# Performance work log

Measured on AMD Instinct MI355X. Metric: run time of the kernel, lower is better.

## Reference

```python
import jax, jax.numpy as jnp
import numpy as np

N = 50000      # nodes
E = 800000     # edges
F_IN = 256     # input node features
H = 64         # hidden_dim
C = 10         # num_classes
G = 64         # graphs in batch


def setup_inputs() -> dict:
    key = jax.random.key(0)
    ks = jax.random.split(key, 10)
    x = jax.random.normal(ks[0], (N, F_IN), dtype=jnp.float32)
    edge_index = jax.random.randint(ks[1], (2, E), 0, N, dtype=jnp.int64)
    batch = jnp.sort(jax.random.randint(ks[2], (N,), 0, G, dtype=jnp.int64))
    def glorot(k, fan_in, fan_out):
        return jax.random.normal(k, (fan_in, fan_out), dtype=jnp.float32) / jnp.sqrt(jnp.float32(fan_in))
    return {
        "x": x,
        "edge_index": edge_index,
        "batch": batch,
        "W1": glorot(ks[3], F_IN, H), "b1": jnp.zeros((H,), jnp.float32),
        "W2": glorot(ks[4], H, H),    "b2": jnp.zeros((H,), jnp.float32),
        "W3": glorot(ks[5], H, H),    "b3": jnp.zeros((H,), jnp.float32),
        "lin_W": glorot(ks[6], H, C), "lin_b": jnp.zeros((C,), jnp.float32),
    }


def reference(x, edge_index, batch, W1, b1, W2, b2, W3, b3, lin_W, lin_b):
    src, dst = edge_index[0], edge_index[1]
    # GCN normalization with self-loops: deg counts (A + I) in-degree
    deg = jax.ops.segment_sum(jnp.ones((E,), x.dtype), dst, num_segments=N) + 1.0
    dis = jax.lax.rsqrt(deg)                       # deg^{-1/2}, [N]
    edge_norm = dis[src] * dis[dst]                # [E]
    self_norm = dis * dis                          # [N] (self-loop weight)

    def gcn_conv_relu(h, W, b):
        h = h @ W                                  # [N, H]
        msg = h[src] * edge_norm[:, None]          # gather + scale, [E, H]
        agg = jax.ops.segment_sum(msg, dst, num_segments=N)
        agg = agg + h * self_norm[:, None]         # self-loop contribution
        return jax.nn.relu(agg + b)                # dropout is identity in eval

    h = gcn_conv_relu(x, W1, b1)
    h = gcn_conv_relu(h, W2, b2)
    h = gcn_conv_relu(h, W3, b3)

    # global mean pool over graphs
    counts = jax.ops.segment_sum(jnp.ones((N,), h.dtype), batch, num_segments=G)
    pooled = jax.ops.segment_sum(h, batch, num_segments=G) / jnp.maximum(counts, 1.0)[:, None]
    return pooled @ lin_W + lin_b                  # [G, C]
```

## Files before the change

### kernel.cpp

```cpp
#include <hip/hip_runtime.h>

#define N_NODES 50000
#define N_EDGES 800000
#define F_INPUT 256
#define HDIM 64
#define NCLS 10
#define NGRAPH 64

#define BSHIFT 7
#define NBUCK 391
#define SCAP 4096

typedef float f32x4v __attribute__((ext_vector_type(4)));
typedef short bf16x8 __attribute__((ext_vector_type(8)));

union B8U { uint4 q; bf16x8 v; };

__device__ __forceinline__ float bflo(unsigned v) { return __uint_as_float(v << 16); }
__device__ __forceinline__ float bfhi(unsigned v) { return __uint_as_float(v & 0xFFFF0000u); }
__device__ __forceinline__ unsigned f2b2(float a, float b) {
    unsigned x = __float_as_uint(a); x = (x + 0x7FFF + ((x >> 16) & 1)) >> 16;
    unsigned y = __float_as_uint(b); y = (y + 0x7FFF + ((y >> 16) & 1)) >> 16;
    return x | (y << 16);
}

__device__ __forceinline__ void split2(float x0, float x1, unsigned& h, unsigned& l) {
    unsigned u0 = __float_as_uint(x0), u1 = __float_as_uint(x1);
    unsigned m0 = u0 & 0xFFFF0000u, m1 = u1 & 0xFFFF0000u;
    h = (u0 >> 16) | m1;
    float r0 = x0 - __uint_as_float(m0);
    float r1 = x1 - __uint_as_float(m1);
    l = (__float_as_uint(r0) >> 16) | (__float_as_uint(r1) & 0xFFFF0000u);
}

__global__ __launch_bounds__(256) void k_part(const int* __restrict__ src,
                                              const int* __restrict__ dst,
                                              int* __restrict__ bcnt,
                                              int* __restrict__ stage, int E) {
    __shared__ int cnt[NBUCK];
    __shared__ int base[NBUCK];
    const int tid = threadIdx.x;
    const int e0 = blockIdx.x * 4096;
    int pb[16], pv[16];
    for (int t = tid; t < NBUCK; t += 256) cnt[t] = 0;
    __syncthreads();
#pragma unroll
    for (int j = 0; j < 16; ++j) {
        int e = e0 + j * 256 + tid;
        if (e < E) {
            int s = src[e], d = dst[e];
            pb[j] = d >> BSHIFT;
            pv[j] = (s << BSHIFT) | (d & 127);
            atomicAdd(&cnt[pb[j]], 1);
        } else pb[j] = -1;
    }
    __syncthreads();
    for (int t = tid; t < NBUCK; t += 256) {
        int c = cnt[t];
        base[t] = c ? atomicAdd(&bcnt[t], c) : 0;
        cnt[t] = 0;
    }
    __syncthreads();
#pragma unroll
    for (int j = 0; j < 16; ++j) {
        if (pb[j] >= 0) {
            int r = base[pb[j]] + atomicAdd(&cnt[pb[j]], 1);
            if (r < SCAP) stage[pb[j] * SCAP + r] = pv[j];
        }
    }
}

__global__ __launch_bounds__(256) void k_csr(const int* __restrict__ stage,
                                             const int* __restrict__ bcnt,
                                             int* __restrict__ degi,
                                             float* __restrict__ dis,
                                             int* __restrict__ off,
                                             int* __restrict__ eadj, int n) {
    __shared__ int cnt[128];
    __shared__ int loc[128];
    __shared__ int lcur[128];
    __shared__ int ebuf[SCAP];
    const int b = blockIdx.x;
    const int tid = threadIdx.x;
    const int n0 = b << BSHIFT;
    const int nn = min(128, n - n0);
    const int sb = b * SCAP;
    const int len = min(bcnt[b], SCAP);
    if (tid < 128) cnt[tid] = 0;
    __syncthreads();
    for (int j = tid; j < len; j += 256) atomicAdd(&cnt[stage[sb + j] & 127], 1);
    __syncthreads();
    if (tid < nn) {
        int dg = cnt[tid];
        degi[n0 + tid] = dg;
        dis[n0 + tid] = rsqrtf((float)(dg + 1));
    }
    if (tid < 128) loc[tid] = cnt[tid];
    __syncthreads();
    for (int d = 1; d < 128; d <<= 1) {
        int x = 0;
        if (tid < 128 && tid >= d) x = loc[tid - d];
        __syncthreads();
        if (tid < 128) loc[tid] += x;
        __syncthreads();
    }
    if (tid < 128) {
        int ex = loc[tid] - cnt[tid];
        if (tid < nn) off[n0 + tid] = sb + ex;
        lcur[tid] = ex;
    }
    __syncthreads();
    for (int j = tid; j < len; j += 256) {
        int p = stage[sb + j];
        int rk = atomicAdd(&lcur[p & 127], 1);
        ebuf[rk] = p >> BSHIFT;
    }
    __syncthreads();
    for (int j = tid; j < len; j += 256) eadj[sb + j] = ebuf[j];
}

__global__ __launch_bounds__(256) void k_prepW(const float* __restrict__ W1,
                                               const float* __restrict__ W2,
                                               const float* __restrict__ W3,
                                               uint4* __restrict__ Bf1,
                                               uint4* __restrict__ Bf2,
                                               uint4* __restrict__ Bf3) {
    int s = blockIdx.x * 256 + threadIdx.x;
    const float* W; uint4* out; int local, KS;
    if (s < 2048)      { W = W1; out = Bf1; local = s;        KS = 8; }
    else if (s < 2560) { W = W2; out = Bf2; local = s - 2048; KS = 2; }
    else               { W = W3; out = Bf3; local = s - 2560; KS = 2; }
    const int lane = local & 63;
    const int t    = (local >> 6) & 3;
    const int ks   = local >> 8;
    const int kb   = ks * 32 + ((lane >> 4) << 3);
    const int col  = t * 16 + (lane & 15);
    unsigned h[4], l[4];
#pragma unroll
    for (int j = 0; j < 4; ++j) {
        float x0 = W[(size_t)(kb + 2 * j) * HDIM + col];
        float x1 = W[(size_t)(kb + 2 * j + 1) * HDIM + col];
        split2(x0, x1, h[j], l[j]);
    }
    out[(ks * 4 + t) * 64 + lane]          = make_uint4(h[0], h[1], h[2], h[3]);
    out[((KS + ks) * 4 + t) * 64 + lane]   = make_uint4(l[0], l[1], l[2], l[3]);
}

__global__ __launch_bounds__(256) void k_gemm_mf(const float* __restrict__ A,
                                                 const uint4* __restrict__ Bf,
                                                 unsigned short* __restrict__ C,
                                                 int n, int lda, int ktn) {
    const int tid = threadIdx.x;
    const int ln  = tid & 63;
    const int wv  = tid >> 6;
    const int m   = ln & 15;
    const int kg  = ln >> 4;
    const int grow = blockIdx.x * 64 + wv * 16 + m;
    const float* ar = A + (size_t)min(grow, n - 1) * lda + kg * 8;

    f32x4v acc[4];
#pragma unroll
    for (int t = 0; t < 4; ++t)
#pragma unroll
        for (int j = 0; j < 4; ++j) acc[t][j] = 0.0f;

    float4 c0 = *(const float4*)(ar);
    float4 c1 = *(const float4*)(ar + 4);

    for (int ks = 0; ks < ktn; ++ks) {
        const int kn = (ks + 1 < ktn) ? (ks + 1) * 32 : 0;
        float4 p0 = *(const float4*)(ar + kn);
        float4 p1 = *(const float4*)(ar + kn + 4);

        const uint4* bp = Bf + (size_t)ks * 256 + ln;
        const uint4* bq = Bf + (size_t)(ktn + ks) * 256 + ln;
        B8U bh0, bh1, bh2, bh3, bl0, bl1, bl2, bl3;
        bh0.q = bp[0];   bh1.q = bp[64];  bh2.q = bp[128]; bh3.q = bp[192];
        bl0.q = bq[0];   bl1.q = bq[64];  bl2.q = bq[128]; bl3.q = bq[192];

        B8U ah, al;
        split2(c0.x, c0.y, ah.q.x, al.q.x);
        split2(c0.z, c0.w, ah.q.y, al.q.y);
        split2(c1.x, c1.y, ah.q.z, al.q.z);
        split2(c1.z, c1.w, ah.q.w, al.q.w);

        acc[0] = __builtin_amdgcn_mfma_f32_16x16x32_bf16(bh0.v, ah.v, acc[0], 0, 0, 0);
        acc[1] = __builtin_amdgcn_mfma_f32_16x16x32_bf16(bh1.v, ah.v, acc[1], 0, 0, 0);
        acc[2] = __builtin_amdgcn_mfma_f32_16x16x32_bf16(bh2.v, ah.v, acc[2], 0, 0, 0);
        acc[3] = __builtin_amdgcn_mfma_f32_16x16x32_bf16(bh3.v, ah.v, acc[3], 0, 0, 0);
        acc[0] = __builtin_amdgcn_mfma_f32_16x16x32_bf16(bl0.v, ah.v, acc[0], 0, 0, 0);
        acc[1] = __builtin_amdgcn_mfma_f32_16x16x32_bf16(bl1.v, ah.v, acc[1], 0, 0, 0);
        acc[2] = __builtin_amdgcn_mfma_f32_16x16x32_bf16(bl2.v, ah.v, acc[2], 0, 0, 0);
        acc[3] = __builtin_amdgcn_mfma_f32_16x16x32_bf16(bl3.v, ah.v, acc[3], 0, 0, 0);
        acc[0] = __builtin_amdgcn_mfma_f32_16x16x32_bf16(bh0.v, al.v, acc[0], 0, 0, 0);
        acc[1] = __builtin_amdgcn_mfma_f32_16x16x32_bf16(bh1.v, al.v, acc[1], 0, 0, 0);
        acc[2] = __builtin_amdgcn_mfma_f32_16x16x32_bf16(bh2.v, al.v, acc[2], 0, 0, 0);
        acc[3] = __builtin_amdgcn_mfma_f32_16x16x32_bf16(bh3.v, al.v, acc[3], 0, 0, 0);

        c0 = p0; c1 = p1;
    }

    if (grow < n) {
#pragma unroll
        for (int t = 0; t < 4; ++t) {
            uint2 p;
            p.x = f2b2(acc[t][0], acc[t][1]);
            p.y = f2b2(acc[t][2], acc[t][3]);
            *(uint2*)(C + (size_t)grow * HDIM + t * 16 + kg * 4) = p;
        }
    }
}

__global__ __launch_bounds__(256) void k_gemm_mb(const unsigned short* __restrict__ A,
                                                 const uint4* __restrict__ Bf,
                                                 unsigned short* __restrict__ C, int n) {
    const int tid = threadIdx.x;
    const int ln  = tid & 63;
    const int wv  = tid >> 6;
    const int m   = ln & 15;
    const int kg  = ln >> 4;
    const int grow = blockIdx.x * 64 + wv * 16 + m;
    const unsigned short* ar = A + (size_t)min(grow, n - 1) * HDIM + kg * 8;

    f32x4v acc[4];
#pragma unroll
    for (int t = 0; t < 4; ++t)
#pragma unroll
        for (int j = 0; j < 4; ++j) acc[t][j] = 0.0f;

#pragma unroll
    for (int ks = 0; ks < 2; ++ks) {
        B8U af;
        af.q = *(const uint4*)(ar + ks * 32);
        const uint4* bp = Bf + ks * 256 + ln;
        const uint4* bq = Bf + (2 + ks) * 256 + ln;
        B8U bh0, bh1, bh2, bh3, bl0, bl1, bl2, bl3;
        bh0.q = bp[0];  bh1.q = bp[64];  bh2.q = bp[128]; bh3.q = bp[192];
        bl0.q = bq[0];  bl1.q = bq[64];  bl2.q = bq[128]; bl3.q = bq[192];

        acc[0] = __builtin_amdgcn_mfma_f32_16x16x32_bf16(bh0.v, af.v, acc[0], 0, 0, 0);
        acc[1] = __builtin_amdgcn_mfma_f32_16x16x32_bf16(bh1.v, af.v, acc[1], 0, 0, 0);
        acc[2] = __builtin_amdgcn_mfma_f32_16x16x32_bf16(bh2.v, af.v, acc[2], 0, 0, 0);
        acc[3] = __builtin_amdgcn_mfma_f32_16x16x32_bf16(bh3.v, af.v, acc[3], 0, 0, 0);
        acc[0] = __builtin_amdgcn_mfma_f32_16x16x32_bf16(bl0.v, af.v, acc[0], 0, 0, 0);
        acc[1] = __builtin_amdgcn_mfma_f32_16x16x32_bf16(bl1.v, af.v, acc[1], 0, 0, 0);
        acc[2] = __builtin_amdgcn_mfma_f32_16x16x32_bf16(bl2.v, af.v, acc[2], 0, 0, 0);
        acc[3] = __builtin_amdgcn_mfma_f32_16x16x32_bf16(bl3.v, af.v, acc[3], 0, 0, 0);
    }

    if (grow < n) {
#pragma unroll
        for (int t = 0; t < 4; ++t) {
            uint2 p;
            p.x = f2b2(acc[t][0], acc[t][1]);
            p.y = f2b2(acc[t][2], acc[t][3]);
            *(uint2*)(C + (size_t)grow * HDIM + t * 16 + kg * 4) = p;
        }
    }
}

__global__ __launch_bounds__(256) void k_gather_b(const unsigned short* __restrict__ h,
                                                  const int* __restrict__ off,
                                                  const int* __restrict__ degi,
                                                  const int* __restrict__ eadj,
                                                  const float* __restrict__ dis,
                                                  const float* __restrict__ bias,
                                                  unsigned short* __restrict__ out, int n) {
    int t = blockIdx.x * 256 + threadIdx.x;
    int i = t >> 3;
    if (i >= n) return;
    const int l8 = t & 7;
    const int q = l8 * 8;
    const int gb = (threadIdx.x & 63) & ~7;
    float di = dis[i];
    int e0 = off[i];
    int e1 = e0 + degi[i];
    float a0 = 0.f, a1 = 0.f, a2 = 0.f, a3 = 0.f, a4 = 0.f, a5 = 0.f, a6 = 0.f, a7 = 0.f;
    for (int base = e0; base < e1; base += 8) {
        const int myE = base + l8;
        int sv = 0; float wv = 0.f;
        if (myE < e1) { sv = eadj[myE]; wv = dis[sv] * di; }
        const int m = e1 - base;
#pragma unroll
        for (int j = 0; j < 8; ++j) {
            if (j < m) {
                int sj = __shfl(sv, gb + j, 64);
                float wj = __shfl(wv, gb + j, 64);
                uint4 u = *(const uint4*)(h + (size_t)sj * HDIM + q);
                a0 = fmaf(bflo(u.x), wj, a0); a1 = fmaf(bfhi(u.x), wj, a1);
                a2 = fmaf(bflo(u.y), wj, a2); a3 = fmaf(bfhi(u.y), wj, a3);
                a4 = fmaf(bflo(u.z), wj, a4); a5 = fmaf(bfhi(u.z), wj, a5);
                a6 = fmaf(bflo(u.w), wj, a6); a7 = fmaf(bfhi(u.w), wj, a7);
            }
        }
    }
    float sn = di * di;
    uint4 us = *(const uint4*)(h + (size_t)i * HDIM + q);
    float4 bl = *(const float4*)(bias + q);
    float4 bh = *(const float4*)(bias + q + 4);
    a0 = fmaxf(fmaf(bflo(us.x), sn, a0) + bl.x, 0.f);
    a1 = fmaxf(fmaf(bfhi(us.x), sn, a1) + bl.y, 0.f);
    a2 = fmaxf(fmaf(bflo(us.y), sn, a2) + bl.z, 0.f);
    a3 = fmaxf(fmaf(bfhi(us.y), sn, a3) + bl.w, 0.f);
    a4 = fmaxf(fmaf(bflo(us.z), sn, a4) + bh.x, 0.f);
    a5 = fmaxf(fmaf(bfhi(us.z), sn, a5) + bh.y, 0.f);
    a6 = fmaxf(fmaf(bflo(us.w), sn, a6) + bh.z, 0.f);
    a7 = fmaxf(fmaf(bfhi(us.w), sn, a7) + bh.w, 0.f);
    uint4 o;
    o.x = f2b2(a0, a1); o.y = f2b2(a2, a3);
    o.z = f2b2(a4, a5); o.w = f2b2(a6, a7);
    *(uint4*)(out + (size_t)i * HDIM + q) = o;
}

__global__ __launch_bounds__(256) void k_gather_pool(const unsigned short* __restrict__ h,
                                                     const int* __restrict__ off,
                                                     const int* __restrict__ degi,
                                                     const int* __restrict__ eadj,
                                                     const float* __restrict__ dis,
                                                     const float* __restrict__ bias,
                                                     const int* __restrict__ batch,
                                                     float* __restrict__ pooled, int n) {
    __shared__ float sp[NGRAPH][HDIM];
    const int tid = threadIdx.x;
    int t = blockIdx.x * 256 + tid;
    int i = t >> 3;
    const bool valid = (i < n);
    const int l8 = t & 7;
    int q = l8 * 8;
    const int gb = (tid & 63) & ~7;
    const int i0 = (blockIdx.x * 256) >> 3;
    const int i1 = min(i0 + 32, n);
    const int gmin = batch[min(i0, n - 1)];
    const int gmax = batch[i1 - 1];
    for (int j = tid; j < NGRAPH * HDIM; j += 256) ((float*)sp)[j] = 0.f;
    __syncthreads();
    if (valid) {
        float di = dis[i];
        int e0 = off[i];
        int e1 = e0 + degi[i];
        float a0 = 0.f, a1 = 0.f, a2 = 0.f, a3 = 0.f, a4 = 0.f, a5 = 0.f, a6 = 0.f, a7 = 0.f;
        for (int base = e0; base < e1; base += 8) {
            const int myE = base + l8;
            int sv = 0; float wv = 0.f;
            if (myE < e1) { sv = eadj[myE]; wv = dis[sv] * di; }
            const int m = e1 - base;
#pragma unroll
            for (int j = 0; j < 8; ++j) {
                if (j < m) {
                    int sj = __shfl(sv, gb + j, 64);
                    float wj = __shfl(wv, gb + j, 64);
                    uint4 u = *(const uint4*)(h + (size_t)sj * HDIM + q);
                    a0 = fmaf(bflo(u.x), wj, a0); a1 = fmaf(bfhi(u.x), wj, a1);
                    a2 = fmaf(bflo(u.y), wj, a2); a3 = fmaf(bfhi(u.y), wj, a3);
                    a4 = fmaf(bflo(u.z), wj, a4); a5 = fmaf(bfhi(u.z), wj, a5);
                    a6 = fmaf(bflo(u.w), wj, a6); a7 = fmaf(bfhi(u.w), wj, a7);
                }
            }
        }
        float sn = di * di;
        uint4 us = *(const uint4*)(h + (size_t)i * HDIM + q);
        float4 bl = *(const float4*)(bias + q);
        float4 bh = *(const float4*)(bias + q + 4);
        a0 = fmaxf(fmaf(bflo(us.x), sn, a0) + bl.x, 0.f);
        a1 = fmaxf(fmaf(bfhi(us.x), sn, a1) + bl.y, 0.f);
        a2 = fmaxf(fmaf(bflo(us.y), sn, a2) + bl.z, 0.f);
        a3 = fmaxf(fmaf(bfhi(us.y), sn, a3) + bl.w, 0.f);
        a4 = fmaxf(fmaf(bflo(us.z), sn, a4) + bh.x, 0.f);
        a5 = fmaxf(fmaf(bfhi(us.z), sn, a5) + bh.y, 0.f);
        a6 = fmaxf(fmaf(bflo(us.w), sn, a6) + bh.z, 0.f);
        a7 = fmaxf(fmaf(bfhi(us.w), sn, a7) + bh.w, 0.f);
        int g = batch[i];
        atomicAdd(&sp[g][q + 0], a0); atomicAdd(&sp[g][q + 1], a1);
        atomicAdd(&sp[g][q + 2], a2); atomicAdd(&sp[g][q + 3], a3);
        atomicAdd(&sp[g][q + 4], a4); atomicAdd(&sp[g][q + 5], a5);
        atomicAdd(&sp[g][q + 6], a6); atomicAdd(&sp[g][q + 7], a7);
    }
    __syncthreads();
    int rows = gmax - gmin + 1;
    for (int j = tid; j < rows * HDIM; j += 256) {
        int r = j >> 6, c = j & 63;
        float v = sp[gmin + r][c];
        if (v != 0.f) atomicAdd(&pooled[(gmin + r) * HDIM + c], v);
    }
}

__global__ __launch_bounds__(640) void k_head(const float* __restrict__ pooled,
                                              const int* __restrict__ batch,
                                              const float* __restrict__ linW,
                                              const float* __restrict__ linb,
                                              float* __restrict__ out, int n) {
    int t = threadIdx.x;
    if (t >= NGRAPH * NCLS) return;
    int g = t / NCLS;
    int c = t - g * NCLS;
    int lo = 0, hi = n;
    while (lo < hi) { int m = (lo + hi) >> 1; if (batch[m] < g) lo = m + 1; else hi = m; }
    int s = lo;
    lo = 0; hi = n;
    while (lo < hi) { int m = (lo + hi) >> 1; if (batch[m] < g + 1) lo = m + 1; else hi = m; }
    float inv = 1.0f / fmaxf((float)(lo - s), 1.0f);
    float acc = linb[c];
#pragma unroll
    for (int k = 0; k < HDIM; ++k)
        acc = fmaf(pooled[g * HDIM + k] * inv, linW[k * NCLS + c], acc);
    out[g * NCLS + c] = acc;
}

extern "C" void kernel_launch(void* const* d_in, const int* in_sizes, int n_in,
                              void* d_out, int out_size, void* d_ws, size_t ws_size,
                              hipStream_t stream) {
    (void)in_sizes; (void)n_in; (void)out_size; (void)ws_size;
    const float* x    = (const float*)d_in[0];
    const int*   ei   = (const int*)d_in[1];
    const int*   batch= (const int*)d_in[2];
    const float* W1   = (const float*)d_in[3];
    const float* b1   = (const float*)d_in[4];
    const float* W2   = (const float*)d_in[5];
    const float* b2   = (const float*)d_in[6];
    const float* W3   = (const float*)d_in[7];
    const float* b3   = (const float*)d_in[8];
    const float* linW = (const float*)d_in[9];
    const float* linb = (const float*)d_in[10];
    float* out = (float*)d_out;

    const int N = N_NODES, E = N_EDGES;
    const int* src = ei;
    const int* dst = ei + E;

    char* ws = (char*)d_ws;
    unsigned short* hA = (unsigned short*)ws; ws += (size_t)N * HDIM * 2;
    unsigned short* hB = (unsigned short*)ws; ws += (size_t)N * HDIM * 2;
    float* dis    = (float*)ws; ws += (size_t)N * 4;
    int*   eadj   = (int*)ws;   ws += (size_t)NBUCK * SCAP * 4;
    int*   stage  = (int*)ws;   ws += (size_t)NBUCK * SCAP * 4;
    int*   degi   = (int*)ws;   ws += (size_t)N * 4;
    int*   off    = (int*)ws;   ws += (size_t)N * 4;
    int*   bcnt   = (int*)ws;   ws += ((size_t)NBUCK * 4 + 15) & ~(size_t)15;
    float* pooled = (float*)ws; ws += (size_t)NGRAPH * HDIM * 4;
    uint4* Bf1    = (uint4*)ws; ws += (size_t)2 * 8 * 4 * 64 * 16;
    uint4* Bf2    = (uint4*)ws; ws += (size_t)2 * 2 * 4 * 64 * 16;
    uint4* Bf3    = (uint4*)ws; ws += (size_t)2 * 2 * 4 * 64 * 16;

    const int nbE = (E + 4095) / 4096;
    const int gb  = (N + 63) / 64;
    const int ngth = (N * 8 + 255) / 256;

    hipMemsetAsync(bcnt, 0, (size_t)NBUCK * 4, stream);
    hipMemsetAsync(pooled, 0, (size_t)NGRAPH * HDIM * 4, stream);
    k_prepW<<<12, 256, 0, stream>>>(W1, W2, W3, Bf1, Bf2, Bf3);
    k_part<<<nbE, 256, 0, stream>>>(src, dst, bcnt, stage, E);
    k_csr<<<NBUCK, 256, 0, stream>>>(stage, bcnt, degi, dis, off, eadj, N);

    k_gemm_mf<<<gb, 256, 0, stream>>>(x, Bf1, hA, N, F_INPUT, 8);
    k_gather_b<<<ngth, 256, 0, stream>>>(hA, off, degi, eadj, dis, b1, hB, N);
    k_gemm_mb<<<gb, 256, 0, stream>>>(hB, Bf2, hA, N);
    k_gather_b<<<ngth, 256, 0, stream>>>(hA, off, degi, eadj, dis, b2, hB, N);
    k_gemm_mb<<<gb, 256, 0, stream>>>(hB, Bf3, hA, N);
    k_gather_pool<<<ngth, 256, 0, stream>>>(hA, off, degi, eadj, dis, b3, batch, pooled, N);
    k_head<<<1, 640, 0, stream>>>(pooled, batch, linW, linb, out, N);
}
```

Before: 256.6 us.

## Precompute per-edge source weights and packed node ranges for SpMM gathers

Adds a per-edge (src, dis[src]) array built by extra blocks appended to the first GEMM launch, and packs each node's edge range and dis into one int4. The gather kernels drop the shuffle-based 8-edge cooperative loop. Instead each lane reads the edge list directly, unrolled by four with two accumulator sets to raise memory-level parallelism. This removes the dependent dis[src] lookup and the shuffles from all three aggregation layers, at the cost of redundant edge-index loads across the 8 lanes of a node and extra workspace traffic.

New measurement: 252.7 us. No clear change (-1.5%).

```diff
diff --git a/kernel.cpp b/kernel.cpp
--- a/kernel.cpp
+++ b/kernel.cpp
@@ -32,6 +32,12 @@
     float r1 = x1 - __uint_as_float(m1);
     l = (__float_as_uint(r0) >> 16) | (__float_as_uint(r1) & 0xFFFF0000u);
 }
+
+#define FMA8(b, u, wt)                                                  \
+    b##0 = fmaf(bflo(u.x), wt, b##0); b##1 = fmaf(bfhi(u.x), wt, b##1); \
+    b##2 = fmaf(bflo(u.y), wt, b##2); b##3 = fmaf(bfhi(u.y), wt, b##3); \
+    b##4 = fmaf(bflo(u.z), wt, b##4); b##5 = fmaf(bfhi(u.z), wt, b##5); \
+    b##6 = fmaf(bflo(u.w), wt, b##6); b##7 = fmaf(bfhi(u.w), wt, b##7);
 
 __global__ __launch_bounds__(256) void k_part(const int* __restrict__ src,
                                               const int* __restrict__ dst,
@@ -72,9 +78,8 @@
 
 __global__ __launch_bounds__(256) void k_csr(const int* __restrict__ stage,
                                              const int* __restrict__ bcnt,
-                                             int* __restrict__ degi,
                                              float* __restrict__ dis,
-                                             int* __restrict__ off,
+                                             int4* __restrict__ rng,
                                              int* __restrict__ eadj, int n) {
     __shared__ int cnt[128];
     __shared__ int loc[128];
@@ -90,11 +95,6 @@
     __syncthreads();
     for (int j = tid; j < len; j += 256) atomicAdd(&cnt[stage[sb + j] & 127], 1);
     __syncthreads();
-    if (tid < nn) {
-        int dg = cnt[tid];
-        degi[n0 + tid] = dg;
-        dis[n0 + tid] = rsqrtf((float)(dg + 1));
-    }
     if (tid < 128) loc[tid] = cnt[tid];
     __syncthreads();
     for (int d = 1; d < 128; d <<= 1) {
@@ -106,7 +106,12 @@
     }
     if (tid < 128) {
         int ex = loc[tid] - cnt[tid];
-        if (tid < nn) off[n0 + tid] = sb + ex;
+        if (tid < nn) {
+            int dg = cnt[tid];
+            float di = rsqrtf((float)(dg + 1));
+            dis[n0 + tid] = di;
+            rng[n0 + tid] = make_int4(sb + ex, sb + ex + dg, __float_as_int(di), 0);
+        }
         lcur[tid] = ex;
     }
     __syncthreads();
@@ -146,10 +151,25 @@
     out[((KS + ks) * 4 + t) * 64 + lane]   = make_uint4(l[0], l[1], l[2], l[3]);
 }
 
-__global__ __launch_bounds__(256) void k_gemm_mf(const float* __restrict__ A,
-                                                 const uint4* __restrict__ Bf,
-                                                 unsigned short* __restrict__ C,
-                                                 int n, int lda, int ktn) {
+__global__ __launch_bounds__(256) void k_gemm_wgt(const float* __restrict__ A,
+                                                  const uint4* __restrict__ Bf,
+                                                  unsigned short* __restrict__ C,
+                                                  int n, int lda, int ktn,
+                                                  const int* __restrict__ eadj,
+                                                  const int* __restrict__ bcnt,
+                                                  const float* __restrict__ dis,
+                                                  int2* __restrict__ ew, int gbN) {
+    if ((int)blockIdx.x >= gbN) {
+        const int b = blockIdx.x - gbN;
+        const int sb = b * SCAP;
+        const int len = min(bcnt[b], SCAP);
+#pragma unroll 4
+        for (int j = threadIdx.x; j < len; j += 256) {
+            int s = eadj[sb + j];
+            ew[sb + j] = make_int2(s, __float_as_int(dis[s]));
+        }
+        return;
+    }
     const int tid = threadIdx.x;
     const int ln  = tid & 63;
     const int wv  = tid >> 6;
@@ -260,40 +280,46 @@
 }
 
 __global__ __launch_bounds__(256) void k_gather_b(const unsigned short* __restrict__ h,
-                                                  const int* __restrict__ off,
-                                                  const int* __restrict__ degi,
-                                                  const int* __restrict__ eadj,
-                                                  const float* __restrict__ dis,
+                                                  const int2* __restrict__ ew,
+                                                  const int4* __restrict__ rng,
                                                   const float* __restrict__ bias,
                                                   unsigned short* __restrict__ out, int n) {
     int t = blockIdx.x * 256 + threadIdx.x;
     int i = t >> 3;
     if (i >= n) return;
-    const int l8 = t & 7;
-    const int q = l8 * 8;
-    const int gb = (threadIdx.x & 63) & ~7;
-    float di = dis[i];
-    int e0 = off[i];
-    int e1 = e0 + degi[i];
+    const int q = (t & 7) * 8;
+    const int4 r = rng[i];
+    int e = r.x; const int e1 = r.y;
+    const float di = __int_as_float(r.z);
     float a0 = 0.f, a1 = 0.f, a2 = 0.f, a3 = 0.f, a4 = 0.f, a5 = 0.f, a6 = 0.f, a7 = 0.f;
-    for (int base = e0; base < e1; base += 8) {
-        const int myE = base + l8;
-        int sv = 0; float wv = 0.f;
-        if (myE < e1) { sv = eadj[myE]; wv = dis[sv] * di; }
-        const int m = e1 - base;
-#pragma unroll
-        for (int j = 0; j < 8; ++j) {
-            if (j < m) {
-                int sj = __shfl(sv, gb + j, 64);
-                float wj = __shfl(wv, gb + j, 64);
-                uint4 u = *(const uint4*)(h + (size_t)sj * HDIM + q);
-                a0 = fmaf(bflo(u.x), wj, a0); a1 = fmaf(bfhi(u.x), wj, a1);
-                a2 = fmaf(bflo(u.y), wj, a2); a3 = fmaf(bfhi(u.y), wj, a3);
-                a4 = fmaf(bflo(u.z), wj, a4); a5 = fmaf(bfhi(u.z), wj, a5);
-                a6 = fmaf(bflo(u.w), wj, a6); a7 = fmaf(bfhi(u.w), wj, a7);
-            }
-        }
-    }
+    float g0 = 0.f, g1 = 0.f, g2 = 0.f, g3 = 0.f, g4 = 0.f, g5 = 0.f, g6 = 0.f, g7 = 0.f;
+#pragma unroll 2
+    for (; e + 3 < e1; e += 4) {
+        int2 w0 = ew[e];
+        int2 w1 = ew[e + 1];
+        int2 w2 = ew[e + 2];
+        int2 w3 = ew[e + 3];
+        uint4 u0 = *(const uint4*)(h + (size_t)w0.x * HDIM + q);
+        uint4 u1 = *(const uint4*)(h + (size_t)w1.x * HDIM + q);
+        uint4 u2 = *(const uint4*)(h + (size_t)w2.x * HDIM + q);
+        uint4 u3 = *(const uint4*)(h + (size_t)w3.x * HDIM + q);
+        float f0 = __int_as_float(w0.y) * di;
+        float f1 = __int_as_float(w1.y) * di;
+        float f2 = __int_as_float(w2.y) * di;
+        float f3 = __int_as_float(w3.y) * di;
+        FMA8(a, u0, f0)
+        FMA8(g, u1, f1)
+        FMA8(a, u2, f2)
+        FMA8(g, u3, f3)
+    }
+    for (; e < e1; ++e) {
+        int2 w0 = ew[e];
+        uint4 u0 = *(const uint4*)(h + (size_t)w0.x * HDIM + q);
+        float f0 = __int_as_float(w0.y) * di;
+        FMA8(a, u0, f0)
+    }
+    a0 += g0; a1 += g1; a2 += g2; a3 += g3;
+    a4 += g4; a5 += g5; a6 += g6; a7 += g7;
     float sn = di * di;
     uint4 us = *(const uint4*)(h + (size_t)i * HDIM + q);
     float4 bl = *(const float4*)(bias + q);
@@ -313,10 +339,8 @@
 }
 
 __global__ __launch_bounds__(256) void k_gather_pool(const unsigned short* __restrict__ h,
-                                                     const int* __restrict__ off,
-                                                     const int* __restrict__ degi,
-                                                     const int* __restrict__ eadj,
-                                                     const float* __restrict__ dis,
+                                                     const int2* __restrict__ ew,
+                                                     const int4* __restrict__ rng,
                                                      const float* __restrict__ bias,
                                                      const int* __restrict__ batch,
                                                      float* __restrict__ pooled, int n) {
@@ -325,9 +349,7 @@
     int t = blockIdx.x * 256 + tid;
     int i = t >> 3;
     const bool valid = (i < n);
-    const int l8 = t & 7;
-    int q = l8 * 8;
-    const int gb = (tid & 63) & ~7;
+    int q = (t & 7) * 8;
     const int i0 = (blockIdx.x * 256) >> 3;
     const int i1 = min(i0 + 32, n);
     const int gmin = batch[min(i0, n - 1)];
@@ -335,28 +357,38 @@
     for (int j = tid; j < NGRAPH * HDIM; j += 256) ((float*)sp)[j] = 0.f;
     __syncthreads();
     if (valid) {
-        float di = dis[i];
-        int e0 = off[i];
-        int e1 = e0 + degi[i];
+        const int4 r = rng[i];
+        int e = r.x; const int e1 = r.y;
+        const float di = __int_as_float(r.z);
         float a0 = 0.f, a1 = 0.f, a2 = 0.f, a3 = 0.f, a4 = 0.f, a5 = 0.f, a6 = 0.f, a7 = 0.f;
-        for (int base = e0; base < e1; base += 8) {
-            const int myE = base + l8;
-            int sv = 0; float wv = 0.f;
-            if (myE < e1) { sv = eadj[myE]; wv = dis[sv] * di; }
-            const int m = e1 - base;
-#pragma unroll
-            for (int j = 0; j < 8; ++j) {
-                if (j < m) {
-                    int sj = __shfl(sv, gb + j, 64);
-                    float wj = __shfl(wv, gb + j, 64);
-                    uint4 u = *(const uint4*)(h + (size_t)sj * HDIM + q);
-                    a0 = fmaf(bflo(u.x), wj, a0); a1 = fmaf(bfhi(u.x), wj, a1);
-                    a2 = fmaf(bflo(u.y), wj, a2); a3 = fmaf(bfhi(u.y), wj, a3);
-                    a4 = fmaf(bflo(u.z), wj, a4); a5 = fmaf(bfhi(u.z), wj, a5);
-                    a6 = fmaf(bflo(u.w), wj, a6); a7 = fmaf(bfhi(u.w), wj, a7);
-                }
-            }
-        }
+        float g0 = 0.f, g1 = 0.f, g2 = 0.f, g3 = 0.f, g4 = 0.f, g5 = 0.f, g6 = 0.f, g7 = 0.f;
+#pragma unroll 2
+        for (; e + 3 < e1; e += 4) {
+            int2 w0 = ew[e];
+            int2 w1 = ew[e + 1];
+            int2 w2 = ew[e + 2];
+            int2 w3 = ew[e + 3];
+            uint4 u0 = *(const uint4*)(h + (size_t)w0.x * HDIM + q);
+            uint4 u1 = *(const uint4*)(h + (size_t)w1.x * HDIM + q);
+            uint4 u2 = *(const uint4*)(h + (size_t)w2.x * HDIM + q);
+            uint4 u3 = *(const uint4*)(h + (size_t)w3.x * HDIM + q);
+            float f0 = __int_as_float(w0.y) * di;
+            float f1 = __int_as_float(w1.y) * di;
+            float f2 = __int_as_float(w2.y) * di;
+            float f3 = __int_as_float(w3.y) * di;
+            FMA8(a, u0, f0)
+            FMA8(g, u1, f1)
+            FMA8(a, u2, f2)
+            FMA8(g, u3, f3)
+        }
+        for (; e < e1; ++e) {
+            int2 w0 = ew[e];
+            uint4 u0 = *(const uint4*)(h + (size_t)w0.x * HDIM + q);
+            float f0 = __int_as_float(w0.y) * di;
+            FMA8(a, u0, f0)
+        }
+        a0 += g0; a1 += g1; a2 += g2; a3 += g3;
+        a4 += g4; a5 += g5; a6 += g6; a7 += g7;
         float sn = di * di;
         uint4 us = *(const uint4*)(h + (size_t)i * HDIM + q);
         float4 bl = *(const float4*)(bias + q);
@@ -433,8 +465,8 @@
     float* dis    = (float*)ws; ws += (size_t)N * 4;
     int*   eadj   = (int*)ws;   ws += (size_t)NBUCK * SCAP * 4;
     int*   stage  = (int*)ws;   ws += (size_t)NBUCK * SCAP * 4;
-    int*   degi   = (int*)ws;   ws += (size_t)N * 4;
-    int*   off    = (int*)ws;   ws += (size_t)N * 4;
+    int2*  ew     = (int2*)ws;  ws += (size_t)NBUCK * SCAP * 8;
+    int4*  rng    = (int4*)ws;  ws += (size_t)N * 16;
     int*   bcnt   = (int*)ws;   ws += ((size_t)NBUCK * 4 + 15) & ~(size_t)15;
     float* pooled = (float*)ws; ws += (size_t)NGRAPH * HDIM * 4;
     uint4* Bf1    = (uint4*)ws; ws += (size_t)2 * 8 * 4 * 64 * 16;
@@ -449,13 +481,14 @@
     hipMemsetAsync(pooled, 0, (size_t)NGRAPH * HDIM * 4, stream);
     k_prepW<<<12, 256, 0, stream>>>(W1, W2, W3, Bf1, Bf2, Bf3);
     k_part<<<nbE, 256, 0, stream>>>(src, dst, bcnt, stage, E);
-    k_csr<<<NBUCK, 256, 0, stream>>>(stage, bcnt, degi, dis, off, eadj, N);
-
-    k_gemm_mf<<<gb, 256, 0, stream>>>(x, Bf1, hA, N, F_INPUT, 8);
-    k_gather_b<<<ngth, 256, 0, stream>>>(hA, off, degi, eadj, dis, b1, hB, N);
+    k_csr<<<NBUCK, 256, 0, stream>>>(stage, bcnt, dis, rng, eadj, N);
+
+    k_gemm_wgt<<<gb + NBUCK, 256, 0, stream>>>(x, Bf1, hA, N, F_INPUT, 8,
+                                               eadj, bcnt, dis, ew, gb);
+    k_gather_b<<<ngth, 256, 0, stream>>>(hA, ew, rng, b1, hB, N);
     k_gemm_mb<<<gb, 256, 0, stream>>>(hB, Bf2, hA, N);
-    k_gather_b<<<ngth, 256, 0, stream>>>(hA, off, degi, eadj, dis, b2, hB, N);
+    k_gather_b<<<ngth, 256, 0, stream>>>(hA, ew, rng, b2, hB, N);
     k_gemm_mb<<<gb, 256, 0, stream>>>(hB, Bf3, hA, N);
-    k_gather_pool<<<ngth, 256, 0, stream>>>(hA, off, degi, eadj, dis, b3, batch, pooled, N);
+    k_gather_pool<<<ngth, 256, 0, stream>>>(hA, ew, rng, b3, batch, pooled, N);
     k_head<<<1, 640, 0, stream>>>(pooled, batch, linW, linb, out, N);
 }
```
